# Kernel optimization log

Measured on AMD Instinct MI355X. Metric: run time of the kernel, lower is better.

The kernel has to match this reference:

```python
import jax, jax.numpy as jnp
import numpy as np

B, S, H, V, C = 32, 512, 256, 50000, 5
NUM_LAYERS, WINDOW = 2, 2


def setup_inputs() -> dict:
    key = jax.random.key(0)
    ks = jax.random.split(key, 24)
    std = 0.1  # matches nn.init.normal_(p, 0, 0.1)
    n = lambda k, shp: jax.random.normal(k, shp, dtype=jnp.float32) * std
    u = lambda k, shp: -0.05 + jax.random.uniform(k, shp, dtype=jnp.float32) * 0.1
    return {
        "input_sentences": jax.random.randint(ks[0], (B, S), 0, V),
        "sentences_length": jax.random.randint(ks[1], (B,), 1, S),
        "hh0": u(ks[2], (B, S, H)),
        "cs0": u(ks[3], (B, S, H)),
        "embed": n(ks[4], (V, H)),
        # stacked word-gate weights, gate order: i, l, r, f, s, output, u
        "W_lr": n(ks[5], (7, H, 2 * H)),
        "W_c": n(ks[6], (7, H, H)),
        "W_x": n(ks[7], (7, H, H)),
        "W_g": n(ks[8], (7, H, H)),
        "gate_bias": n(ks[9], (7, H)),
        # sentence-state gates
        "W_fg_g": n(ks[10], (H, H)),
        "W_fg_h": n(ks[11], (H, H)),
        "W_fgi_g": n(ks[12], (H, H)),
        "W_fgi_h": n(ks[13], (H, H)),
        "W_og_g": n(ks[14], (H, H)),
        "W_og_h": n(ks[15], (H, H)),
        "b_fg": n(ks[16], (H,)),
        "b_fgi": n(ks[17], (H,)),
        # output head
        "W1": n(ks[18], (H, 2 * H)),
        "b1": n(ks[19], (H,)),
        "Wout": n(ks[20], (C, H)),
        "bout": n(ks[21], (C,)),
    }


def _before_sum(x, window):
    # sum of right-shifted (zero-padded at front) copies, shifts 1..window
    out = jnp.zeros_like(x)
    for s in range(1, window + 1):
        out = out + jnp.pad(x[:, :-s], ((0, 0), (s, 0), (0, 0)))
    return out


def _after_sum(x, window):
    out = jnp.zeros_like(x)
    for s in range(1, window + 1):
        out = out + jnp.pad(x[:, s:], ((0, 0), (0, s), (0, 0)))
    return out


def _slstm_step(hh, cs, sv, scs, wv, W_lr, W_c, W_x, W_g, gate_bias,
                W_fg_g, W_fg_h, W_fgi_g, W_fgi_h, W_og_g, W_og_h, b_fg, b_fgi):
    avg_hh = hh.mean(axis=1)                                   # [B,H]
    f_hat_g = jax.nn.sigmoid(sv @ W_fg_g.T + avg_hh @ W_fg_h.T + b_fg)
    # NOTE: original code (faithfully) uses output_gate_bias here, not output_gate_g_bias
    og_g = jax.nn.sigmoid(sv @ W_og_g.T + avg_hh @ W_og_h.T + gate_bias[5])
    f_hat_g_i = jax.nn.sigmoid((sv @ W_fgi_g.T)[:, None] + hh @ W_fgi_h.T + b_fgi)
    scores = jax.nn.softmax(f_hat_g_i, axis=2)                 # over hidden dim
    new_scs = jax.nn.softmax(f_hat_g, axis=1) * scs + (scores * cs).sum(axis=1)
    new_sv = og_g * jnp.tanh(new_scs)

    hb = _before_sum(hh, WINDOW)
    ha = _after_sum(hh, WINDOW)
    cb = _before_sum(cs, WINDOW)
    ca = _after_sum(cs, WINDOW)
    ba = jnp.concatenate([hb, ha], axis=-1)                    # [B,S,2H]

    # all 7 gate pre-activations at once: [B,S,7,H]
    pre = (jnp.einsum('bsk,ghk->bsgh', ba, W_lr)
           + jnp.einsum('bsk,ghk->bsgh', hh, W_c)
           + jnp.einsum('bsk,ghk->bsgh', wv, W_x)
           + (jnp.einsum('bk,ghk->bgh', new_sv, W_g) + gate_bias)[:, None])

    g5 = jax.nn.sigmoid(pre[..., :5, :])                       # i,l,r,f,s
    b_, s_ = g5.shape[:2]
    # joint softmax over the concatenated 5*H gate vector (as in torch cat+softmax)
    g5 = jax.nn.softmax(g5.reshape(b_, s_, -1), axis=-1).reshape(b_, s_, 5, -1)
    i_t, l_t, r_t, f_t, s_t = (g5[..., k, :] for k in range(5))
    og = jax.nn.sigmoid(pre[..., 5, :])
    u_g = jnp.tanh(pre[..., 6, :])

    new_cs = l_t * cb + f_t * cs + r_t * ca + s_t * scs[:, None] + i_t * u_g
    new_hh = og * jnp.tanh(new_cs)
    return new_hh, new_cs, new_sv, new_scs


def reference(input_sentences, sentences_length, hh0, cs0, embed,
              W_lr, W_c, W_x, W_g, gate_bias,
              W_fg_g, W_fg_h, W_fgi_g, W_fgi_h, W_og_g, W_og_h, b_fg, b_fgi,
              W1, b1, Wout, bout):
    wv = embed[input_sentences]                                # [B,S,H]
    hh, cs = hh0, cs0
    sv, scs = hh0.mean(axis=1), cs0.mean(axis=1)
    for _ in range(NUM_LAYERS):
        hh, cs, sv, scs = _slstm_step(hh, cs, sv, scs, wv,
                                      W_lr, W_c, W_x, W_g, gate_bias,
                                      W_fg_g, W_fg_h, W_fgi_g, W_fgi_h,
                                      W_og_g, W_og_h, b_fg, b_fgi)
    avg_hh = hh.mean(axis=1)
    conc = jnp.concatenate([avg_hh, sv], axis=1) @ W1.T + b1
    fc = conc @ Wout.T + bout
    return jax.nn.log_softmax(fc, axis=1), sv
```

## Files before the change

### kernel.cpp

```cpp
#include <hip/hip_runtime.h>
#include <stdint.h>
#include <math.h>

#define B_   32
#define S_   512
#define H_   256
#define M_   (B_*S_)
#define KBIG 1024
#define NB   1792
#define NB2  2048
#define C_   5

typedef __bf16 bf16;
typedef __bf16 bf16x4 __attribute__((ext_vector_type(4)));
typedef __bf16 bf16x8 __attribute__((ext_vector_type(8)));
typedef float  floatx4 __attribute__((ext_vector_type(4)));

__device__ __forceinline__ float sigm(float x){ return 1.f/(1.f+expf(-x)); }

__device__ __forceinline__ void gl16(const bf16* g, bf16* l){
    __builtin_amdgcn_global_load_lds(
        (const __attribute__((address_space(1))) unsigned int*)g,
        (__attribute__((address_space(3))) unsigned int*)l, 16, 0, 0);
}

__global__ void wcomb_k(const float* __restrict__ Wlr, const float* __restrict__ Wc,
                        const float* __restrict__ Wx, const float* __restrict__ Wfgi,
                        bf16* __restrict__ WT){
    int n = blockIdx.x;
    int k4 = threadIdx.x * 4;
    float4 v;
    if (n < NB){
        int g = n >> 8, h = n & 255;
        const float* src;
        if (k4 < 512)      src = Wlr + ((size_t)(g*256 + h))*512 + k4;
        else if (k4 < 768) src = Wc  + ((size_t)(g*256 + h))*256 + (k4 - 512);
        else               src = Wx  + ((size_t)(g*256 + h))*256 + (k4 - 768);
        v = *(const float4*)src;
    } else {
        int h = n - NB;
        if (k4 >= 512 && k4 < 768) v = *(const float4*)(Wfgi + (size_t)h*H_ + (k4 - 512));
        else { v.x=0.f; v.y=0.f; v.z=0.f; v.w=0.f; }
    }
    bf16 o[4] = {(bf16)v.x,(bf16)v.y,(bf16)v.z,(bf16)v.w};
    *(uint2*)&WT[(size_t)n*KBIG + k4] = *(uint2*)o;
}

__global__ void gather_k(const int* __restrict__ idx, const float* __restrict__ embed,
                         bf16* __restrict__ X){
    int i4 = (blockIdx.x*256 + threadIdx.x)*4;
    int m = i4 >> 8, h = i4 & 255;
    float4 v = *(const float4*)(embed + (size_t)idx[m]*H_ + h);
    bf16 o[4] = {(bf16)v.x,(bf16)v.y,(bf16)v.z,(bf16)v.w};
    *(uint2*)(X + (size_t)m*KBIG + 768 + h) = *(uint2*)o;
}

__global__ void mean1_k(const float* __restrict__ x, float* __restrict__ part){
    int b = blockIdx.x, c = blockIdx.y, h = threadIdx.x;
    const float* p = x + ((size_t)b*S_ + c*32)*H_ + h;
    float s = 0.f;
    #pragma unroll 8
    for (int t=0;t<32;t++) s += p[(size_t)t*H_];
    part[((size_t)b*16 + c)*H_ + h] = s;
}
__global__ void mean2_k(const float* __restrict__ part, float* __restrict__ out){
    int b = blockIdx.x, h = threadIdx.x;
    float s = 0.f;
    #pragma unroll
    for (int c=0;c<16;c++) s += part[((size_t)b*16 + c)*H_ + h];
    out[b*H_ + h] = s * (1.f/512.f);
}

__global__ void buildx_k(const float* __restrict__ hh, bf16* __restrict__ X){
    int m = blockIdx.x, tid = threadIdx.x;
    int seg = tid >> 6, li = tid & 63;
    int s = m & (S_-1);
    int h0 = li*4;
    size_t base = (size_t)m*H_ + h0;
    bf16* xr = X + (size_t)m*KBIG + seg*H_ + h0;
    const float4 z = {0.f,0.f,0.f,0.f};
    float4 v;
    if (seg == 0){
        float4 a = (s>=1) ? *(const float4*)&hh[base - H_]   : z;
        float4 b = (s>=2) ? *(const float4*)&hh[base - 2*H_] : z;
        v.x=a.x+b.x; v.y=a.y+b.y; v.z=a.z+b.z; v.w=a.w+b.w;
    } else if (seg == 1){
        float4 a = (s<=S_-2) ? *(const float4*)&hh[base + H_]   : z;
        float4 b = (s<=S_-3) ? *(const float4*)&hh[base + 2*H_] : z;
        v.x=a.x+b.x; v.y=a.y+b.y; v.z=a.z+b.z; v.w=a.w+b.w;
    } else {
        v = *(const float4*)&hh[base];
    }
    bf16 o[4] = {(bf16)v.x,(bf16)v.y,(bf16)v.z,(bf16)v.w};
    *(uint2*)xr = *(uint2*)o;
}

__global__ void mv5_k(const float* __restrict__ sv, const float* __restrict__ avg,
    const float* __restrict__ Wfg_g, const float* __restrict__ Wfg_h,
    const float* __restrict__ Wog_g, const float* __restrict__ Wog_h,
    const float* __restrict__ Wfgi_g, float* __restrict__ res){
    int j = blockIdx.x, b = blockIdx.y, h = threadIdx.x;
    const float* vec = (j==1 || j==3) ? avg + b*H_ : sv + b*H_;
    const float* W   = (j==0)?Wfg_g:(j==1)?Wfg_h:(j==2)?Wog_g:(j==3)?Wog_h:Wfgi_g;
    __shared__ float v[H_];
    v[h] = vec[h]; __syncthreads();
    const float* w = W + (size_t)h*H_;
    float d = 0.f;
    for (int k=0;k<H_;k++) d += v[k]*w[k];
    res[((size_t)b*5 + j)*H_ + h] = d;
}
__global__ void comb_k(const float* __restrict__ res, const float* __restrict__ b_fg,
                       const float* __restrict__ gbias, const float* __restrict__ b_fgi,
                       float* __restrict__ fhg, float* __restrict__ ogg,
                       float* __restrict__ svg){
    int b = blockIdx.x, h = threadIdx.x;
    const float* r = res + (size_t)b*5*H_;
    fhg[b*H_+h] = sigm(r[h] + r[H_+h] + b_fg[h]);
    ogg[b*H_+h] = sigm(r[2*H_+h] + r[3*H_+h] + gbias[5*H_+h]);
    svg[b*H_+h] = r[4*H_+h] + b_fgi[h];
}

__device__ __forceinline__ void mmq(floatx4 (&acc)[8][4], bf16x8 (&af)[4][2], bf16x8 (&bfr)[2][2],
                                    int MH, int NH){
    #pragma unroll
    for (int mi2=0;mi2<4;mi2++)
        #pragma unroll
        for (int ni2=0;ni2<2;ni2++)
            #pragma unroll
            for (int kk=0;kk<2;kk++)
                acc[MH*4+mi2][NH*2+ni2] = __builtin_amdgcn_mfma_f32_16x16x32_bf16(
                    af[mi2][kk], bfr[ni2][kk], acc[MH*4+mi2][NH*2+ni2], 0, 0, 0);
}

__global__ __launch_bounds__(512, 2)
void mgemm256_k(const bf16* __restrict__ A, const bf16* __restrict__ BT,
                bf16* __restrict__ C, int Kdim, int lda, int ldb, int ldc, int nbx){
    __shared__ alignas(16) bf16 lsA[2][256*64];
    __shared__ alignas(16) bf16 lsB[2][256*64];
    const int tid  = threadIdx.x;
    const int lane = tid & 63;
    const int wave = tid >> 6;
    const int wm = wave >> 2;
    const int wn = wave & 3;
    const int lrow = lane & 15, quad = lane >> 4;

    const int cpx = gridDim.x >> 3;
    const int w   = (blockIdx.x & 7)*cpx + (blockIdx.x >> 3);
    const int mb  = w / nbx, nb = w - mb*nbx;
    const int m0 = mb * 256, n0 = nb * 256;

    const int srow = tid >> 3;
    const int scol = ((tid & 7) ^ (srow & 7)) * 8;
    const bf16* Ab = A  + (size_t)(m0 + srow)*lda + scol;
    const bf16* Bb = BT + (size_t)(n0 + srow)*ldb + scol;
    const int NT = Kdim >> 6;

    floatx4 zero = {0.f,0.f,0.f,0.f};
    floatx4 acc[8][4];
    #pragma unroll
    for (int i=0;i<8;i++)
        #pragma unroll
        for (int j=0;j<4;j++) acc[i][j] = zero;
    bf16x8 af[4][2], bfrA[2][2], bfrB[2][2];

#define SA_(bu,r,kt) gl16(Ab + (size_t)(r)*64*lda + (size_t)(kt)*64, &lsA[bu][(r)*4096 + tid*8])
#define SB_(bu,r,kt) gl16(Bb + (size_t)(r)*64*ldb + (size_t)(kt)*64, &lsB[bu][(r)*4096 + tid*8])
#define RA_(bu,MH,mi2,kk) (*(const bf16x8*)&lsA[bu][(wm*128 + (MH)*64 + (mi2)*16 + lrow)*64 + ((((kk)*4+quad) ^ (lrow&7))*8)])
#define RB_(bu,NH,ni2,kk) (*(const bf16x8*)&lsB[bu][(wn*64  + (NH)*32 + (ni2)*16 + lrow)*64 + ((((kk)*4+quad) ^ (lrow&7))*8)])

    SB_(0,0,0); SB_(0,1,0); SB_(0,2,0); SB_(0,3,0);
    SA_(0,0,0); SA_(0,2,0); SA_(0,1,0); SA_(0,3,0);
    asm volatile("s_waitcnt vmcnt(2)" ::: "memory");
    __builtin_amdgcn_s_barrier();

    for (int kt = 0; kt < NT; ++kt){
        const int cur = kt & 1, nxt = cur ^ 1;
        const bool st = (kt + 1 < NT);
        const int k1 = kt + 1;

        #pragma unroll
        for (int mi2=0;mi2<4;mi2++){ af[mi2][0] = RA_(cur,0,mi2,0); af[mi2][1] = RA_(cur,0,mi2,1); }
        #pragma unroll
        for (int ni2=0;ni2<2;ni2++){ bfrA[ni2][0] = RB_(cur,0,ni2,0); bfrA[ni2][1] = RB_(cur,0,ni2,1); }
        if (st){ SB_(nxt,0,k1); SB_(nxt,1,k1); }
        __builtin_amdgcn_s_barrier();
        __builtin_amdgcn_s_setprio(1);
        mmq(acc, af, bfrA, 0, 0);
        __builtin_amdgcn_s_setprio(0);
        __builtin_amdgcn_s_barrier();

        #pragma unroll
        for (int ni2=0;ni2<2;ni2++){ bfrB[ni2][0] = RB_(cur,1,ni2,0); bfrB[ni2][1] = RB_(cur,1,ni2,1); }
        if (st){ SB_(nxt,2,k1); SB_(nxt,3,k1); }
        __builtin_amdgcn_s_barrier();
        __builtin_amdgcn_s_setprio(1);
        mmq(acc, af, bfrB, 0, 1);
        __builtin_amdgcn_s_setprio(0);
        if (st) asm volatile("s_waitcnt vmcnt(4)" ::: "memory");
        else    asm volatile("s_waitcnt vmcnt(0)" ::: "memory");
        __builtin_amdgcn_s_barrier();

        #pragma unroll
        for (int mi2=0;mi2<4;mi2++){ af[mi2][0] = RA_(cur,1,mi2,0); af[mi2][1] = RA_(cur,1,mi2,1); }
        if (st){ SA_(nxt,0,k1); SA_(nxt,2,k1); }
        __builtin_amdgcn_s_barrier();
        __builtin_amdgcn_s_setprio(1);
        mmq(acc, af, bfrB, 1, 1);
        __builtin_amdgcn_s_setprio(0);
        __builtin_amdgcn_s_barrier();

        if (st){ SA_(nxt,1,k1); SA_(nxt,3,k1); }
        __builtin_amdgcn_s_barrier();
        __builtin_amdgcn_s_setprio(1);
        mmq(acc, af, bfrA, 1, 0);
        __builtin_amdgcn_s_setprio(0);
        if (st) asm volatile("s_waitcnt vmcnt(2)" ::: "memory");
        __builtin_amdgcn_s_barrier();
    }
#undef SA_
#undef SB_
#undef RA_
#undef RB_

    #pragma unroll
    for (int mi=0;mi<8;mi++)
        #pragma unroll
        for (int ni=0;ni<4;ni++){
            int row = m0 + wm*128 + mi*16 + quad*4;
            int col = n0 + wn*64  + ni*16 + lrow;
            #pragma unroll
            for (int r=0;r<4;r++)
                C[(size_t)(row+r)*ldc + col] = (bf16)acc[mi][ni][r];
        }
}

__global__ void scorep_k(const bf16* __restrict__ fgih, const float* __restrict__ svg,
                         const float* __restrict__ cs, float* __restrict__ part, int ldf){
    int chunk = blockIdx.x, b = blockIdx.y;
    int tid = threadIdx.x, wave = tid >> 6, lane = tid & 63;
    __shared__ float acc4[4][256];
    int h0 = lane*4;
    float4 swv = *(const float4*)&svg[b*H_ + h0];
    float sw[4] = {swv.x, swv.y, swv.z, swv.w};
    float acc[4] = {0.f,0.f,0.f,0.f};
    for (int t=wave; t<16; t+=4){
        int m = b*S_ + chunk*16 + t;
        bf16x4 fv = *(const bf16x4*)&fgih[(size_t)m*ldf + h0];
        float e[4], loc = 0.f;
        #pragma unroll
        for (int j=0;j<4;j++){ e[j] = expf(sigm(sw[j] + (float)fv[j])); loc += e[j]; }
        #pragma unroll
        for (int off=32; off; off>>=1) loc += __shfl_xor(loc, off, 64);
        float inv = 1.f/loc;
        float4 cv = *(const float4*)&cs[(size_t)m*H_ + h0];
        acc[0] += e[0]*inv*cv.x; acc[1] += e[1]*inv*cv.y;
        acc[2] += e[2]*inv*cv.z; acc[3] += e[3]*inv*cv.w;
    }
    #pragma unroll
    for (int j=0;j<4;j++) acc4[wave][h0+j] = acc[j];
    __syncthreads();
    part[((size_t)b*32 + chunk)*H_ + tid] =
        acc4[0][tid] + acc4[1][tid] + acc4[2][tid] + acc4[3][tid];
}

__global__ void newscs_k(const float* __restrict__ part, const float* __restrict__ fhg,
                         const float* __restrict__ ogg, const float* __restrict__ scs_in,
                         float* __restrict__ scs_out, float* __restrict__ sv_out){
    int b = blockIdx.x, h = threadIdx.x;
    __shared__ float r[256];
    float dot = 0.f;
    #pragma unroll 8
    for (int c=0;c<32;c++) dot += part[((size_t)b*32+c)*H_ + h];
    float e = expf(fhg[b*H_+h]);
    r[h] = e; __syncthreads();
    for (int off=128; off; off>>=1){ if (h<off) r[h] += r[h+off]; __syncthreads(); }
    float ns = (e / r[0]) * scs_in[b*H_+h] + dot;
    scs_out[b*H_+h] = ns;
    sv_out[b*H_+h]  = ogg[b*H_+h] * tanhf(ns);
}

__global__ void gterm_k(const float* __restrict__ svn, const float* __restrict__ Wg,
                        const float* __restrict__ gbias, float* __restrict__ gt){
    int g = blockIdx.x, b = blockIdx.y, h = threadIdx.x;
    __shared__ float s[H_];
    s[h] = svn[b*H_+h]; __syncthreads();
    const float* w = Wg + ((size_t)g*H_ + h)*H_;
    float d = 0.f;
    for (int k=0;k<H_;k++) d += s[k]*w[k];
    gt[(size_t)b*NB + g*H_ + h] = d + gbias[g*H_+h];
}

__global__ void gates_k(const bf16* __restrict__ pre, const float* __restrict__ gt,
                        const float* __restrict__ cs_in, const float* __restrict__ scs_in,
                        float* __restrict__ hh_out, float* __restrict__ cs_out,
                        bf16* __restrict__ Xn, int ldp){
    int tid = threadIdx.x, wave = tid >> 6, lane = tid & 63;
    int m = blockIdx.x*4 + wave;
    int b = m >> 9, s = m & (S_-1);
    const bf16* row = pre + (size_t)m*ldp;
    int h0 = lane*4;
    float pv[7][4];
    #pragma unroll
    for (int g=0; g<7; ++g){
        bf16x4 t = *(const bf16x4*)&row[g*H_ + h0];
        float4 gq = *(const float4*)&gt[(size_t)b*NB + g*H_ + h0];
        pv[g][0] = (float)t[0] + gq.x;
        pv[g][1] = (float)t[1] + gq.y;
        pv[g][2] = (float)t[2] + gq.z;
        pv[g][3] = (float)t[3] + gq.w;
    }
    float ex[5][4], og[4], u[4];
    float loc = 0.f;
    #pragma unroll
    for (int g=0; g<5; ++g)
        #pragma unroll
        for (int j=0;j<4;j++){ float e = expf(sigm(pv[g][j])); ex[g][j] = e; loc += e; }
    #pragma unroll
    for (int j=0;j<4;j++){ og[j] = sigm(pv[5][j]); u[j] = tanhf(pv[6][j]); }
    #pragma unroll
    for (int off=32; off; off>>=1) loc += __shfl_xor(loc, off, 64);
    float inv = 1.f / loc;

    size_t i0 = (size_t)m*H_ + h0;
    const float4 z = {0.f,0.f,0.f,0.f};
    float4 c0  = *(const float4*)&cs_in[i0];
    float4 cm1 = (s>=1)    ? *(const float4*)&cs_in[i0 - H_]   : z;
    float4 cm2 = (s>=2)    ? *(const float4*)&cs_in[i0 - 2*H_] : z;
    float4 cp1 = (s<=S_-2) ? *(const float4*)&cs_in[i0 + H_]   : z;
    float4 cp2 = (s<=S_-3) ? *(const float4*)&cs_in[i0 + 2*H_] : z;
    float4 sc  = *(const float4*)&scs_in[(size_t)b*H_ + h0];
    float4 nc4, nh4;
    #pragma unroll
    for (int j=0;j<4;j++){
        float cb = ((const float*)&cm1)[j] + ((const float*)&cm2)[j];
        float ca = ((const float*)&cp1)[j] + ((const float*)&cp2)[j];
        float nc = ex[1][j]*inv*cb + ex[3][j]*inv*((const float*)&c0)[j] + ex[2][j]*inv*ca
                 + ex[4][j]*inv*((const float*)&sc)[j] + ex[0][j]*inv*u[j];
        ((float*)&nc4)[j] = nc;
        ((float*)&nh4)[j] = og[j] * tanhf(nc);
    }
    *(float4*)&cs_out[i0] = nc4;
    *(float4*)&hh_out[i0] = nh4;
    if (Xn){
        bf16 o[4] = {(bf16)((float*)&nh4)[0], (bf16)((float*)&nh4)[1],
                     (bf16)((float*)&nh4)[2], (bf16)((float*)&nh4)[3]};
        *(uint2*)&Xn[(size_t)m*KBIG + 512 + h0] = *(uint2*)o;
    }
}

__global__ void head_k(const float* __restrict__ avgh, const float* __restrict__ sv,
                       const float* __restrict__ W1, const float* __restrict__ b1,
                       const float* __restrict__ Wout, const float* __restrict__ bout,
                       float* __restrict__ out){
    int b = blockIdx.x, t = threadIdx.x;
    __shared__ float conc[H_];
    __shared__ float fc[8];
    const float* wr = W1 + (size_t)t*512;
    float d = b1[t];
    for (int k=0;k<H_;k++) d += avgh[b*H_+k]*wr[k];
    for (int k=0;k<H_;k++) d += sv[b*H_+k]*wr[256+k];
    conc[t] = d;
    __syncthreads();
    if (t < C_){
        const float* wo = Wout + (size_t)t*H_;
        float s = bout[t];
        for (int i=0;i<H_;i++) s += conc[i]*wo[i];
        fc[t] = s;
    }
    __syncthreads();
    if (t == 0){
        float mx = fc[0];
        for (int c=1;c<C_;c++) mx = fmaxf(mx, fc[c]);
        float se = 0.f;
        for (int c=0;c<C_;c++) se += expf(fc[c]-mx);
        float lse = mx + logf(se);
        for (int c=0;c<C_;c++) out[b*C_+c] = fc[c]-lse;
    }
    out[B_*C_ + b*H_ + t] = sv[b*H_+t];
}

extern "C" void kernel_launch(void* const* d_in, const int* in_sizes, int n_in,
                              void* d_out, int out_size, void* d_ws, size_t ws_size,
                              hipStream_t stream){
    const int*   idx    = (const int*)d_in[0];
    const float* hh0    = (const float*)d_in[2];
    const float* cs0    = (const float*)d_in[3];
    const float* embed  = (const float*)d_in[4];
    const float* Wlr    = (const float*)d_in[5];
    const float* Wc     = (const float*)d_in[6];
    const float* Wx     = (const float*)d_in[7];
    const float* Wg     = (const float*)d_in[8];
    const float* gbias  = (const float*)d_in[9];
    const float* Wfg_g  = (const float*)d_in[10];
    const float* Wfg_h  = (const float*)d_in[11];
    const float* Wfgi_g = (const float*)d_in[12];
    const float* Wfgi_h = (const float*)d_in[13];
    const float* Wog_g  = (const float*)d_in[14];
    const float* Wog_h  = (const float*)d_in[15];
    const float* b_fg   = (const float*)d_in[16];
    const float* b_fgi  = (const float*)d_in[17];
    const float* W1     = (const float*)d_in[18];
    const float* b1     = (const float*)d_in[19];
    const float* Wout   = (const float*)d_in[20];
    const float* bout   = (const float*)d_in[21];

    uint8_t* p = (uint8_t*)d_ws;
    auto alloc = [&](size_t bytes)->void*{ void* r=(void*)p; p += (bytes + 255) & ~(size_t)255; return r; };
    bf16*  WT    = (bf16*)alloc((size_t)NB2*KBIG*2);
    bf16*  X     = (bf16*)alloc((size_t)M_*KBIG*2);
    bf16*  pre   = (bf16*)alloc((size_t)M_*NB2*2);
    float* hhA = (float*)alloc((size_t)M_*H_*4);
    float* csA = (float*)alloc((size_t)M_*H_*4);
    float* hhB = (float*)alloc((size_t)M_*H_*4);
    float* csB = (float*)alloc((size_t)M_*H_*4);
    float* mpart= (float*)alloc((size_t)B_*16*H_*4);
    float* part = (float*)alloc((size_t)B_*32*H_*4);
    float* res5 = (float*)alloc((size_t)B_*5*H_*4);
    float* avgh = (float*)alloc(B_*H_*4);
    float* fhg  = (float*)alloc(B_*H_*4);
    float* ogg  = (float*)alloc(B_*H_*4);
    float* svg  = (float*)alloc(B_*H_*4);
    float* svP0 = (float*)alloc(B_*H_*4);
    float* svP1 = (float*)alloc(B_*H_*4);
    float* scP0 = (float*)alloc(B_*H_*4);
    float* scP1 = (float*)alloc(B_*H_*4);
    float* gt   = (float*)alloc((size_t)B_*NB*4);

    wcomb_k <<<NB2,         256, 0, stream>>>(Wlr, Wc, Wx, Wfgi_h, WT);
    gather_k<<<(M_*H_)/1024,256, 0, stream>>>(idx, embed, X);
    mean1_k <<<dim3(B_,16), 256, 0, stream>>>(hh0, mpart);
    mean2_k <<<B_,          256, 0, stream>>>(mpart, svP0);
    mean1_k <<<dim3(B_,16), 256, 0, stream>>>(cs0, mpart);
    mean2_k <<<B_,          256, 0, stream>>>(mpart, scP0);

    const float *hin = hh0, *cin = cs0;
    float *hout = hhA, *cout = csA;
    float *svin = svP0, *scin = scP0, *svout = svP1, *scout = scP1;

    for (int l=0; l<2; ++l){
        const float* avgp;
        if (l == 0){
            avgp = svin;
        } else {
            mean1_k<<<dim3(B_,16), 256, 0, stream>>>(hin, mpart);
            mean2_k<<<B_,          256, 0, stream>>>(mpart, avgh);
            avgp = avgh;
        }
        mv5_k   <<<dim3(5,B_), 256, 0, stream>>>(svin, avgp, Wfg_g, Wfg_h, Wog_g,
                                                 Wog_h, Wfgi_g, res5);
        comb_k  <<<B_, 256, 0, stream>>>(res5, b_fg, gbias, b_fgi, fhg, ogg, svg);
        buildx_k<<<M_, (l==0 ? 192 : 128), 0, stream>>>(hin, X);
        mgemm256_k<<<512, 512, 0, stream>>>(X, WT, pre, KBIG, KBIG, KBIG, NB2, 8);
        scorep_k<<<dim3(32,B_), 256, 0, stream>>>(pre + NB, svg, cin, part, NB2);
        newscs_k<<<B_, 256, 0, stream>>>(part, fhg, ogg, scin, scout, svout);
        gterm_k <<<dim3(7,B_), 256, 0, stream>>>(svout, Wg, gbias, gt);
        gates_k <<<M_/4, 256, 0, stream>>>(pre, gt, cin, scin, hout, cout,
                                           (l==0 ? X : (bf16*)nullptr), NB2);
        hin = hout; cin = cout;
        hout = (l==0) ? hhB : hhA;
        cout = (l==0) ? csB : csA;
        float* q;
        q = svin; svin = svout; svout = q;
        q = scin; scin = scout; scout = q;
    }
    mean1_k<<<dim3(B_,16), 256, 0, stream>>>(hin, mpart);
    mean2_k<<<B_,          256, 0, stream>>>(mpart, avgh);
    head_k <<<B_, 256, 0, stream>>>(avgh, svin, W1, b1, Wout, bout, (float*)d_out);
}
```

Before: 515.4 us.

## Switch GEMM to 4-stage K=32 LDS pipeline with prefetch depth three

```diff
diff --git a/kernel.cpp b/kernel.cpp
--- a/kernel.cpp
+++ b/kernel.cpp
@@ -120,23 +120,11 @@
     svg[b*H_+h] = r[4*H_+h] + b_fgi[h];
 }
 
-__device__ __forceinline__ void mmq(floatx4 (&acc)[8][4], bf16x8 (&af)[4][2], bf16x8 (&bfr)[2][2],
-                                    int MH, int NH){
-    #pragma unroll
-    for (int mi2=0;mi2<4;mi2++)
-        #pragma unroll
-        for (int ni2=0;ni2<2;ni2++)
-            #pragma unroll
-            for (int kk=0;kk<2;kk++)
-                acc[MH*4+mi2][NH*2+ni2] = __builtin_amdgcn_mfma_f32_16x16x32_bf16(
-                    af[mi2][kk], bfr[ni2][kk], acc[MH*4+mi2][NH*2+ni2], 0, 0, 0);
-}
-
 __global__ __launch_bounds__(512, 2)
 void mgemm256_k(const bf16* __restrict__ A, const bf16* __restrict__ BT,
                 bf16* __restrict__ C, int Kdim, int lda, int ldb, int ldc, int nbx){
-    __shared__ alignas(16) bf16 lsA[2][256*64];
-    __shared__ alignas(16) bf16 lsB[2][256*64];
+    __shared__ alignas(16) bf16 lsA[4][256*32];
+    __shared__ alignas(16) bf16 lsB[4][256*32];
     const int tid  = threadIdx.x;
     const int lane = tid & 63;
     const int wave = tid >> 6;
@@ -149,11 +137,11 @@
     const int mb  = w / nbx, nb = w - mb*nbx;
     const int m0 = mb * 256, n0 = nb * 256;
 
-    const int srow = tid >> 3;
-    const int scol = ((tid & 7) ^ (srow & 7)) * 8;
+    const int srow = tid >> 2;
+    const int scol = (tid & 3) * 8;
     const bf16* Ab = A  + (size_t)(m0 + srow)*lda + scol;
     const bf16* Bb = BT + (size_t)(n0 + srow)*ldb + scol;
-    const int NT = Kdim >> 6;
+    const int NT = Kdim >> 5;
 
     floatx4 zero = {0.f,0.f,0.f,0.f};
     floatx4 acc[8][4];
@@ -161,60 +149,43 @@
     for (int i=0;i<8;i++)
         #pragma unroll
         for (int j=0;j<4;j++) acc[i][j] = zero;
-    bf16x8 af[4][2], bfrA[2][2], bfrB[2][2];
-
-#define SA_(bu,r,kt) gl16(Ab + (size_t)(r)*64*lda + (size_t)(kt)*64, &lsA[bu][(r)*4096 + tid*8])
-#define SB_(bu,r,kt) gl16(Bb + (size_t)(r)*64*ldb + (size_t)(kt)*64, &lsB[bu][(r)*4096 + tid*8])
-#define RA_(bu,MH,mi2,kk) (*(const bf16x8*)&lsA[bu][(wm*128 + (MH)*64 + (mi2)*16 + lrow)*64 + ((((kk)*4+quad) ^ (lrow&7))*8)])
-#define RB_(bu,NH,ni2,kk) (*(const bf16x8*)&lsB[bu][(wn*64  + (NH)*32 + (ni2)*16 + lrow)*64 + ((((kk)*4+quad) ^ (lrow&7))*8)])
-
-    SB_(0,0,0); SB_(0,1,0); SB_(0,2,0); SB_(0,3,0);
-    SA_(0,0,0); SA_(0,2,0); SA_(0,1,0); SA_(0,3,0);
-    asm volatile("s_waitcnt vmcnt(2)" ::: "memory");
-    __builtin_amdgcn_s_barrier();
+    bf16x8 af[8], bfr[4];
+
+#define SA_(bu,r,kt) gl16(Ab + (size_t)(r)*128*lda + (size_t)(kt)*32, &lsA[bu][(r)*4096 + tid*8])
+#define SB_(bu,r,kt) gl16(Bb + (size_t)(r)*128*ldb + (size_t)(kt)*32, &lsB[bu][(r)*4096 + tid*8])
+#define RA_(bu,mi) (*(const bf16x8*)&lsA[bu][(wm*128 + (mi)*16 + lrow)*32 + quad*8])
+#define RB_(bu,ni) (*(const bf16x8*)&lsB[bu][(wn*64  + (ni)*16 + lrow)*32 + quad*8])
+
+    #pragma unroll
+    for (int t=0; t<3; ++t){ SA_(t,0,t); SA_(t,1,t); SB_(t,0,t); SB_(t,1,t); }
 
     for (int kt = 0; kt < NT; ++kt){
-        const int cur = kt & 1, nxt = cur ^ 1;
-        const bool st = (kt + 1 < NT);
-        const int k1 = kt + 1;
-
-        #pragma unroll
-        for (int mi2=0;mi2<4;mi2++){ af[mi2][0] = RA_(cur,0,mi2,0); af[mi2][1] = RA_(cur,0,mi2,1); }
-        #pragma unroll
-        for (int ni2=0;ni2<2;ni2++){ bfrA[ni2][0] = RB_(cur,0,ni2,0); bfrA[ni2][1] = RB_(cur,0,ni2,1); }
-        if (st){ SB_(nxt,0,k1); SB_(nxt,1,k1); }
+        const int cur = kt & 3;
+        const int pf  = kt + 3;
+        if (pf < NT){
+            const int pb = pf & 3;
+            SA_(pb,0,pf); SA_(pb,1,pf); SB_(pb,0,pf); SB_(pb,1,pf);
+        }
+        const int rem = NT - 1 - kt;
+        if (rem >= 3)      asm volatile("s_waitcnt vmcnt(12)" ::: "memory");
+        else if (rem == 2) asm volatile("s_waitcnt vmcnt(8)"  ::: "memory");
+        else if (rem == 1) asm volatile("s_waitcnt vmcnt(4)"  ::: "memory");
+        else               asm volatile("s_waitcnt vmcnt(0)"  ::: "memory");
         __builtin_amdgcn_s_barrier();
+
+        #pragma unroll
+        for (int mi=0;mi<8;mi++) af[mi]  = RA_(cur,mi);
+        #pragma unroll
+        for (int ni=0;ni<4;ni++) bfr[ni] = RB_(cur,ni);
         __builtin_amdgcn_s_setprio(1);
-        mmq(acc, af, bfrA, 0, 0);
+        #pragma unroll
+        for (int mi=0;mi<8;mi++)
+            #pragma unroll
+            for (int ni=0;ni<4;ni++)
+                acc[mi][ni] = __builtin_amdgcn_mfma_f32_16x16x32_bf16(af[mi], bfr[ni], acc[mi][ni], 0, 0, 0);
         __builtin_amdgcn_s_setprio(0);
-        __builtin_amdgcn_s_barrier();
-
-        #pragma unroll
-        for (int ni2=0;ni2<2;ni2++){ bfrB[ni2][0] = RB_(cur,1,ni2,0); bfrB[ni2][1] = RB_(cur,1,ni2,1); }
-        if (st){ SB_(nxt,2,k1); SB_(nxt,3,k1); }
-        __builtin_amdgcn_s_barrier();
-        __builtin_amdgcn_s_setprio(1);
-        mmq(acc, af, bfrB, 0, 1);
-        __builtin_amdgcn_s_setprio(0);
-        if (st) asm volatile("s_waitcnt vmcnt(4)" ::: "memory");
-        else    asm volatile("s_waitcnt vmcnt(0)" ::: "memory");
-        __builtin_amdgcn_s_barrier();
-
-        #pragma unroll
-        for (int mi2=0;mi2<4;mi2++){ af[mi2][0] = RA_(cur,1,mi2,0); af[mi2][1] = RA_(cur,1,mi2,1); }
-        if (st){ SA_(nxt,0,k1); SA_(nxt,2,k1); }
-        __builtin_amdgcn_s_barrier();
-        __builtin_amdgcn_s_setprio(1);
-        mmq(acc, af, bfrB, 1, 1);
-        __builtin_amdgcn_s_setprio(0);
-        __builtin_amdgcn_s_barrier();
-
-        if (st){ SA_(nxt,1,k1); SA_(nxt,3,k1); }
-        __builtin_amdgcn_s_barrier();
-        __builtin_amdgcn_s_setprio(1);
-        mmq(acc, af, bfrA, 1, 0);
-        __builtin_amdgcn_s_setprio(0);
-        if (st) asm volatile("s_waitcnt vmcnt(2)" ::: "memory");
+
+        asm volatile("s_waitcnt lgkmcnt(0)" ::: "memory");
         __builtin_amdgcn_s_barrier();
     }
 #undef SA_
```

Measured after the change: 541.6 us. +5.1%, slower.
